# Kernel tuning notes

Measured on AMD Instinct MI355X. Metric: run time of the kernel, lower is better.

The kernel has to match this reference:

```python
import jax, jax.numpy as jnp
import numpy as np
import math

N_KEYS = 2048      # set size (number of pragma keys)
EMB = 768          # embed_size
KEY_E = 512        # key_embed_size
VAL_E = 256        # val_embed_size (KEY_E + VAL_E == EMB)
CAT_VOCAB = 100000 # categorical embedding rows
N_REG = 1000       # integer-key embedding rows / per-key Linear(1,256) encoders
HID = 512          # hidden_size (dim_V)
HEADS = 8
N_OUT = 7          # PMA num_outputs
SCALE = math.sqrt(HID)  # original divides by sqrt(dim_V), not sqrt(head_dim)


def _split_heads(x):
    # torch: torch.cat(x.split(dim_V//h, 2), 0)  -> [h*B, N, dim_V/h]
    return jnp.concatenate(jnp.split(x, HEADS, axis=2), axis=0)


def _merge_heads(x):
    # torch: torch.cat(x.split(B, 0), 2)
    return jnp.concatenate(jnp.split(x, HEADS, axis=0), axis=2)


def _mab(Q, K, wq, bq, wk, bk, wv, bv, wo, bo):
    # MAB with ln=False: project, head-split along batch, attend, residual, relu FF residual
    Qp = Q @ wq.T + bq
    Kp = K @ wk.T + bk
    Vp = K @ wv.T + bv
    Q_, K_, V_ = _split_heads(Qp), _split_heads(Kp), _split_heads(Vp)
    A = jax.nn.softmax(jnp.einsum('bqd,bkd->bqk', Q_, K_) / SCALE, axis=-1)
    O = _merge_heads(Q_ + jnp.einsum('bqk,bkd->bqd', A, V_))
    return O + jax.nn.relu(O @ wo.T + bo)


def _forward(reg_values, cat_table, reg_table, reg_W, reg_b,
             q0_w, q0_b, k0_w, k0_b, v0_w, v0_b, o0_w, o0_b,
             qs_w, qs_b, ks_w, ks_b, vs_w, vs_b, os_w, os_b,
             S, pq_w, pq_b, pk_w, pk_b, pv_w, pv_b, po_w, po_b,
             fc_w, fc_b, is_cat, cat_idx, reg_idx):
    # vectorized form of the per-key python loop: gather -> tiny linear encode -> select
    val_emb = reg_W[reg_idx] * reg_values[:, None] + reg_b[reg_idx]     # [N, VAL_E]
    reg_full = jnp.concatenate([reg_table[reg_idx], val_emb], axis=-1)  # [N, EMB]
    emb = jnp.where(is_cat[:, None], cat_table[cat_idx], reg_full)[None]  # [1, N, EMB]
    x = _mab(emb, emb, q0_w, q0_b, k0_w, k0_b, v0_w, v0_b, o0_w, o0_b)
    for i in range(3):
        x = _mab(x, x, qs_w[i], qs_b[i], ks_w[i], ks_b[i], vs_w[i], vs_b[i], os_w[i], os_b[i])
    # decoder: PMA (MAB(S, X)) then Linear(HID, 1)
    s = jnp.broadcast_to(S, (x.shape[0], N_OUT, HID))
    p = _mab(s, x, pq_w, pq_b, pk_w, pk_b, pv_w, pv_b, po_w, po_b)      # [1, N_OUT, HID]
    return (p @ fc_w.T + fc_b).reshape(-1)                              # [N_OUT]


def setup_inputs() -> dict:
    key = jax.random.key(0)
    ks = iter(jax.random.split(key, 48))
    def w(shape, s=0.02):
        return jax.random.normal(next(ks), shape, jnp.float32) * s
    inp = {}
    inp['is_cat'] = jax.random.bernoulli(next(ks), 0.5, (N_KEYS,))
    inp['cat_idx'] = jax.random.randint(next(ks), (N_KEYS,), 0, CAT_VOCAB)
    inp['reg_idx'] = jax.random.randint(next(ks), (N_KEYS,), 0, N_REG)
    inp['reg_values'] = jax.random.uniform(next(ks), (N_KEYS,), jnp.float32, 1.0, 64.0)
    inp['cat_table'] = w((CAT_VOCAB, EMB), 0.05)
    inp['reg_table'] = w((N_REG, KEY_E), 0.05)
    inp['reg_W'] = w((N_REG, VAL_E))
    inp['reg_b'] = w((N_REG, VAL_E))
    inp['q0_w'] = w((HID, EMB)); inp['q0_b'] = w((HID,))
    inp['k0_w'] = w((HID, EMB)); inp['k0_b'] = w((HID,))
    inp['v0_w'] = w((HID, EMB)); inp['v0_b'] = w((HID,))
    inp['o0_w'] = w((HID, HID)); inp['o0_b'] = w((HID,))
    for nm in ['qs', 'ks', 'vs', 'os']:
        inp[nm + '_w'] = w((3, HID, HID))
        inp[nm + '_b'] = w((3, HID))
    inp['S'] = w((1, N_OUT, HID), 0.05)
    for nm in ['pq', 'pk', 'pv', 'po']:
        inp[nm + '_w'] = w((HID, HID))
        inp[nm + '_b'] = w((HID,))
    inp['fc_w'] = w((1, HID)); inp['fc_b'] = w((1,))
    return inp


def reference(is_cat, cat_idx, reg_idx, reg_values, cat_table, reg_table, reg_W, reg_b,
              q0_w, q0_b, k0_w, k0_b, v0_w, v0_b, o0_w, o0_b,
              qs_w, qs_b, ks_w, ks_b, vs_w, vs_b, os_w, os_b,
              S, pq_w, pq_b, pk_w, pk_b, pv_w, pv_b, po_w, po_b, fc_w, fc_b):
    return _forward(reg_values, cat_table, reg_table, reg_W, reg_b,
                    q0_w, q0_b, k0_w, k0_b, v0_w, v0_b, o0_w, o0_b,
                    qs_w, qs_b, ks_w, ks_b, vs_w, vs_b, os_w, os_b,
                    S, pq_w, pq_b, pk_w, pk_b, pv_w, pv_b, po_w, po_b,
                    fc_w, fc_b, is_cat, cat_idx, reg_idx)
```

## Files before the change

kernel.cpp:

```cpp
#include <hip/hip_runtime.h>
#include <stdint.h>


#define HID 512
#define EMBD 768
#define NCTX 2048
#define HD 64

typedef __attribute__((ext_vector_type(8))) short v8s;
typedef __attribute__((ext_vector_type(4))) float v4f;

#define MFMA(a, b, c) __builtin_amdgcn_mfma_f32_16x16x32_bf16((a), (b), (c), 0, 0, 0)

__device__ __forceinline__ short f2bf(float f) {
  uint32_t u = __builtin_bit_cast(uint32_t, f);
  uint32_t r = (u + 0x7FFFu + ((u >> 16) & 1u)) >> 16;
  return (short)r;
}
__device__ __forceinline__ float bf2f(short s) {
  uint32_t u = ((uint32_t)(uint16_t)s) << 16;
  return __builtin_bit_cast(float, u);
}
__device__ __forceinline__ v8s ldbf8(const short* p) { return *(const v8s*)p; }

struct ConvDesc {
  const float* src[20];
  unsigned cum[21];
};

__global__ void k_convert(ConvDesc d, short* __restrict__ dst) {
  unsigned i = blockIdx.x * 256u + threadIdx.x;
  if (i >= d.cum[20]) return;
  int t = 0;
  while (i >= d.cum[t + 1]) ++t;
  dst[i] = f2bf(d.src[t][i - d.cum[t]]);
}

__global__ void k_emb(const int* __restrict__ is_cat, const int* __restrict__ cat_idx,
                      const int* __restrict__ reg_idx, const float* __restrict__ reg_values,
                      const float* __restrict__ cat_table, const float* __restrict__ reg_table,
                      const float* __restrict__ reg_W, const float* __restrict__ reg_b,
                      short* __restrict__ out) {
  int i = blockIdx.x * 256 + threadIdx.x;
  int n = i / EMBD, e = i - n * EMBD;
  float v;
  if (is_cat[n]) {
    v = cat_table[(long)cat_idx[n] * EMBD + e];
  } else {
    int r = reg_idx[n];
    if (e < 512) v = reg_table[r * 512 + e];
    else {
      int e2 = e - 512;
      v = reg_W[r * 256 + e2] * reg_values[n] + reg_b[r * 256 + e2];
    }
  }
  out[i] = f2bf(v);
}

__global__ void k_sbuild(const float* __restrict__ S, short* __restrict__ out) {
  int i = blockIdx.x * 256 + threadIdx.x;
  int row = i >> 9;
  out[i] = (row < 7) ? f2bf(S[i]) : (short)0;
}

template <int EPI, int KK>
__global__ __launch_bounds__(64) void k_gemm(const short* __restrict__ A,
                                             const short* __restrict__ B,
                                             const float* __restrict__ biasA,
                                             const float* __restrict__ biasB,
                                             const short* __restrict__ resid,
                                             short* __restrict__ out, int N) {
  int l = threadIdx.x, l16 = l & 15, quad = l >> 4;
  int i0 = blockIdx.y * 16, n0 = blockIdx.x * 64;
  const short* arow = A + (i0 + l16) * KK + quad * 8;
  const short* brow = B + (n0 + l16) * KK + quad * 8;
  v4f acc[4];
  for (int t = 0; t < 4; ++t) acc[t] = (v4f){0.f, 0.f, 0.f, 0.f};
#pragma unroll 2
  for (int k = 0; k < KK; k += 32) {
    v8s a = ldbf8(arow + k);
    acc[0] = MFMA(a, ldbf8(brow + k), acc[0]);
    acc[1] = MFMA(a, ldbf8(brow + 16 * KK + k), acc[1]);
    acc[2] = MFMA(a, ldbf8(brow + 32 * KK + k), acc[2]);
    acc[3] = MFMA(a, ldbf8(brow + 48 * KK + k), acc[3]);
  }
  for (int t = 0; t < 4; ++t) {
    int col = n0 + t * 16 + l16;
    float bc;
    if (EPI == 0) bc = (col < 512) ? biasA[col] : biasB[col - 512];
    else if (EPI == 2) bc = biasA[col];
    else bc = 0.f;
    for (int r = 0; r < 4; ++r) {
      int row = i0 + quad * 4 + r;
      float v = acc[t][r];
      if (EPI == 0) v += bc;
      else if (EPI == 1) v += biasA[row];
      else v = bf2f(resid[row * N + col]) + fmaxf(v + bc, 0.f);
      out[row * N + col] = f2bf(v);
    }
  }
}

__global__ __launch_bounds__(256) void k_flash(const short* __restrict__ Q, int qstride,
                                               const short* __restrict__ Kp, int kstride,
                                               const short* __restrict__ Vt,
                                               short* __restrict__ out) {
  __shared__ __align__(16) short Kt[64 * 64];
  __shared__ __align__(16) short Vtl[64 * 64];
  __shared__ __align__(16) short P[4][16 * 72];
  const int tid = threadIdx.x;
  const int wave = tid >> 6, l = tid & 63, l16 = l & 15, quad = l >> 4;
  const int D0 = blockIdx.y * HD;
  const int i0 = blockIdx.x * 64 + wave * 16;

  const short* qrow = Q + (i0 + l16) * qstride + D0 + quad * 8;
  const v8s aq0 = ldbf8(qrow);
  const v8s aq1 = ldbf8(qrow + 32);

  const int sr = tid >> 2, sc0 = tid & 3, sc1 = sc0 + 4;
  const short* kg = Kp + sr * kstride + D0;
  const short* vg = Vt + (D0 + sr) * NCTX;
  short* kl0 = &Kt[(sr * 8 + (sc0 ^ (sr & 7))) * 8];
  short* kl1 = &Kt[(sr * 8 + (sc1 ^ (sr & 7))) * 8];
  short* vl0 = &Vtl[(sr * 8 + (sc0 ^ (sr & 7))) * 8];
  short* vl1 = &Vtl[(sr * 8 + (sc1 ^ (sr & 7))) * 8];

  v4f o[4];
  float lsum[4];
  for (int t = 0; t < 4; ++t) o[t] = (v4f){0.f, 0.f, 0.f, 0.f};
  for (int r = 0; r < 4; ++r) lsum[r] = 0.f;

  v8s pk0 = ldbf8(kg + sc0 * 8), pk1 = ldbf8(kg + sc1 * 8);
  v8s pv0 = ldbf8(vg + sc0 * 8), pv1 = ldbf8(vg + sc1 * 8);

  const float C2 = 0.06375872f;

  for (int j0 = 0; j0 < NCTX; j0 += 64) {
    __syncthreads();
    *(v8s*)kl0 = pk0; *(v8s*)kl1 = pk1;
    *(v8s*)vl0 = pv0; *(v8s*)vl1 = pv1;
    __syncthreads();
    int jn = j0 + 64;
    if (jn < NCTX) {
      pk0 = ldbf8(kg + jn * kstride + sc0 * 8);
      pk1 = ldbf8(kg + jn * kstride + sc1 * 8);
      pv0 = ldbf8(vg + jn + sc0 * 8);
      pv1 = ldbf8(vg + jn + sc1 * 8);
    }
    v4f s[4];
    for (int kt = 0; kt < 4; ++kt) {
      int R = kt * 16 + l16;
      v8s kb0 = *(const v8s*)&Kt[(R * 8 + (quad ^ (R & 7))) * 8];
      v8s kb1 = *(const v8s*)&Kt[(R * 8 + ((quad + 4) ^ (R & 7))) * 8];
      v4f t0 = (v4f){0.f, 0.f, 0.f, 0.f};
      t0 = MFMA(aq0, kb0, t0);
      s[kt] = MFMA(aq1, kb1, t0);
    }
    short* pw = &P[wave][0];
    for (int kt = 0; kt < 4; ++kt)
      for (int r = 0; r < 4; ++r) {
        float p = exp2f(fminf(s[kt][r] * C2, 40.f));
        lsum[r] += p;
        pw[(quad * 4 + r) * 72 + kt * 16 + l16] = f2bf(p);
      }
    __syncthreads();
    v8s pa0 = *(const v8s*)&pw[l16 * 72 + quad * 8];
    v8s pa1 = *(const v8s*)&pw[l16 * 72 + 32 + quad * 8];
    for (int t = 0; t < 4; ++t) {
      int R = t * 16 + l16;
      v8s bv0 = *(const v8s*)&Vtl[(R * 8 + (quad ^ (R & 7))) * 8];
      v8s bv1 = *(const v8s*)&Vtl[(R * 8 + ((quad + 4) ^ (R & 7))) * 8];
      o[t] = MFMA(pa0, bv0, o[t]);
      o[t] = MFMA(pa1, bv1, o[t]);
    }
  }
  for (int r = 0; r < 4; ++r) {
    lsum[r] += __shfl_xor(lsum[r], 1);
    lsum[r] += __shfl_xor(lsum[r], 2);
    lsum[r] += __shfl_xor(lsum[r], 4);
    lsum[r] += __shfl_xor(lsum[r], 8);
  }
  for (int r = 0; r < 4; ++r) {
    float inv = 1.f / lsum[r];
    int row = i0 + quad * 4 + r;
    for (int t = 0; t < 4; ++t) {
      int col = D0 + t * 16 + l16;
      out[row * HID + col] = f2bf(bf2f(Q[row * qstride + col]) + o[t][r] * inv);
    }
  }
}

__global__ __launch_bounds__(64) void k_fc(const short* __restrict__ P,
                                           const float* __restrict__ fcw,
                                           const float* __restrict__ fcb,
                                           float* __restrict__ out) {
  int j = blockIdx.x, l = threadIdx.x;
  float s = 0.f;
  int d0 = l * 8;
  for (int d = d0; d < d0 + 8; ++d) s += bf2f(P[j * HID + d]) * fcw[d];
  for (int msk = 1; msk < 64; msk <<= 1) s += __shfl_xor(s, msk);
  if (l == 0) out[j] = s + fcb[0];
}

extern "C" void kernel_launch(void* const* d_in, const int* in_sizes, int n_in,
                              void* d_out, int out_size, void* d_ws, size_t ws_size,
                              hipStream_t stream) {
  const int* is_cat = (const int*)d_in[0];
  const int* cat_idx = (const int*)d_in[1];
  const int* reg_idx = (const int*)d_in[2];
  const float* reg_values = (const float*)d_in[3];
  const float* cat_table = (const float*)d_in[4];
  const float* reg_table = (const float*)d_in[5];
  const float* reg_W = (const float*)d_in[6];
  const float* reg_b = (const float*)d_in[7];
  const float* q0_w = (const float*)d_in[8];  const float* q0_b = (const float*)d_in[9];
  const float* k0_w = (const float*)d_in[10]; const float* k0_b = (const float*)d_in[11];
  const float* v0_w = (const float*)d_in[12]; const float* v0_b = (const float*)d_in[13];
  const float* o0_w = (const float*)d_in[14]; const float* o0_b = (const float*)d_in[15];
  const float* qs_w = (const float*)d_in[16]; const float* qs_b = (const float*)d_in[17];
  const float* ks_w = (const float*)d_in[18]; const float* ks_b = (const float*)d_in[19];
  const float* vs_w = (const float*)d_in[20]; const float* vs_b = (const float*)d_in[21];
  const float* os_w = (const float*)d_in[22]; const float* os_b = (const float*)d_in[23];
  const float* S    = (const float*)d_in[24];
  const float* pq_w = (const float*)d_in[25]; const float* pq_b = (const float*)d_in[26];
  const float* pk_w = (const float*)d_in[27]; const float* pk_b = (const float*)d_in[28];
  const float* pv_w = (const float*)d_in[29]; const float* pv_b = (const float*)d_in[30];
  const float* po_w = (const float*)d_in[31]; const float* po_b = (const float*)d_in[32];
  const float* fc_w = (const float*)d_in[33]; const float* fc_b = (const float*)d_in[34];

  short* W = (short*)d_ws;

  const unsigned OWQK[4] = {0u, 1441792u, 2490368u, 3538944u};
  const unsigned OWV[4]  = {786432u, 1966080u, 3014656u, 4063232u};
  const unsigned OWO[4]  = {1179648u, 2228224u, 3276800u, 4325376u};
  const unsigned OPQW = 4587520u, OPKW = 4849664u, OPVW = 5111808u, OPOW = 5373952u;
  const unsigned TOTW = 5636096u;
  const unsigned OEMB = TOTW;
  const unsigned OXA  = OEMB + 1572864u;
  const unsigned OXB  = OXA + 1048576u;
  const unsigned OQK  = OXB + 1048576u;
  const unsigned OVT  = OQK + 2097152u;
  const unsigned OOH  = OVT + 1048576u;
  const unsigned OSB  = OOH + 1048576u;
  const unsigned OQPP = OSB + 32768u;
  const unsigned OKPP = OQPP + 32768u;
  const unsigned OOHP = OKPP + 1048576u;
  const unsigned OPP  = OOHP + 32768u;

  ConvDesc cd;
  const float* srcs[20] = {
      q0_w, k0_w, v0_w, o0_w,
      qs_w, ks_w, vs_w, os_w,
      qs_w + 262144, ks_w + 262144, vs_w + 262144, os_w + 262144,
      qs_w + 524288, ks_w + 524288, vs_w + 524288, os_w + 524288,
      pq_w, pk_w, pv_w, po_w};
  const unsigned cums[21] = {0u,       393216u,  786432u,  1179648u, 1441792u,
                             1703936u, 1966080u, 2228224u, 2490368u, 2752512u,
                             3014656u, 3276800u, 3538944u, 3801088u, 4063232u,
                             4325376u, 4587520u, 4849664u, 5111808u, 5373952u,
                             5636096u};
  for (int i = 0; i < 20; ++i) cd.src[i] = srcs[i];
  for (int i = 0; i < 21; ++i) cd.cum[i] = cums[i];
  k_convert<<<(TOTW + 255) / 256, 256, 0, stream>>>(cd, W);

  k_emb<<<(2048 * 768) / 256, 256, 0, stream>>>(is_cat, cat_idx, reg_idx, reg_values,
                                                cat_table, reg_table, reg_W, reg_b,
                                                W + OEMB);
  k_sbuild<<<(64 * 512) / 256, 256, 0, stream>>>(S, W + OSB);

  const float* bq[4] = {q0_b, qs_b, qs_b + 512, qs_b + 1024};
  const float* bk[4] = {k0_b, ks_b, ks_b + 512, ks_b + 1024};
  const float* bv[4] = {v0_b, vs_b, vs_b + 512, vs_b + 1024};
  const float* bo[4] = {o0_b, os_b, os_b + 512, os_b + 1024};
  const unsigned oxin[4]  = {OEMB, OXA, OXB, OXA};
  const unsigned oxout[4] = {OXA, OXB, OXA, OXB};

  dim3 gqk(16, 128);
  dim3 gv(32, 32);
  dim3 go(8, 128);
  dim3 gf(32, 8);

  for (int l = 0; l < 4; ++l) {
    const short* X = W + oxin[l];
    short* Xout = W + oxout[l];
    if (l == 0) {
      k_gemm<0, 768><<<gqk, 64, 0, stream>>>(X, W + OWQK[0], bq[0], bk[0], nullptr, W + OQK, 1024);
      k_gemm<1, 768><<<gv, 64, 0, stream>>>(W + OWV[0], X, bv[0], bv[0], nullptr, W + OVT, 2048);
    } else {
      k_gemm<0, 512><<<gqk, 64, 0, stream>>>(X, W + OWQK[l], bq[l], bk[l], nullptr, W + OQK, 1024);
      k_gemm<1, 512><<<gv, 64, 0, stream>>>(W + OWV[l], X, bv[l], bv[l], nullptr, W + OVT, 2048);
    }
    k_flash<<<gf, 256, 0, stream>>>(W + OQK, 1024, W + OQK + 512, 1024, W + OVT, W + OOH);
    k_gemm<2, 512><<<go, 64, 0, stream>>>(W + OOH, W + OWO[l], bo[l], bo[l], W + OOH, Xout, 512);
  }

  k_gemm<0, 512><<<dim3(8, 4), 64, 0, stream>>>(W + OSB, W + OPQW, pq_b, pq_b, nullptr, W + OQPP, 512);
  k_gemm<0, 512><<<dim3(8, 128), 64, 0, stream>>>(W + OXB, W + OPKW, pk_b, pk_b, nullptr, W + OKPP, 512);
  k_gemm<1, 512><<<dim3(32, 32), 64, 0, stream>>>(W + OPVW, W + OXB, pv_b, pv_b, nullptr, W + OVT, 2048);
  k_flash<<<dim3(1, 8), 256, 0, stream>>>(W + OQPP, 512, W + OKPP, 512, W + OVT, W + OOHP);
  k_gemm<2, 512><<<dim3(8, 1), 64, 0, stream>>>(W + OOHP, W + OPOW, po_b, po_b, W + OOHP, W + OPP, 512);
  k_fc<<<7, 64, 0, stream>>>(W + OPP, fc_w, fc_b, (float*)d_out);
}
```

Measured before the change: 833.8 us.

## Split attention over key chunks with combine kernel and enlarge GEMM row tiles

The flash attention kernel now splits the 2048-key loop into 4 chunks along a new grid z dimension. Each chunk writes unnormalized fp32 partial outputs and row sums, and a new k_combine kernel sums the partials, normalizes them and adds the residual. This gives four times as many workgroups for a grid that previously filled only about one block per CU. The GEMM kernel now computes 32 rows per wave, two A fragments sharing each B load, which halves the grid sizes and reduces B reloads. The per-wave P buffer handoff uses an LDS waitcnt instead of a block barrier. The cost is an extra launch and fp32 partial traffic per layer.

```diff
diff --git a/kernel.cpp b/kernel.cpp
--- a/kernel.cpp
+++ b/kernel.cpp
@@ -71,55 +71,63 @@
                                              const short* __restrict__ resid,
                                              short* __restrict__ out, int N) {
   int l = threadIdx.x, l16 = l & 15, quad = l >> 4;
-  int i0 = blockIdx.y * 16, n0 = blockIdx.x * 64;
-  const short* arow = A + (i0 + l16) * KK + quad * 8;
-  const short* brow = B + (n0 + l16) * KK + quad * 8;
-  v4f acc[4];
-  for (int t = 0; t < 4; ++t) acc[t] = (v4f){0.f, 0.f, 0.f, 0.f};
-#pragma unroll 2
+  int i0 = blockIdx.y * 32, n0 = blockIdx.x * 64;
+  const short* a0p = A + (i0 + l16) * KK + quad * 8;
+  const short* a1p = a0p + 16 * KK;
+  const short* bp = B + (n0 + l16) * KK + quad * 8;
+  v4f acc[2][4];
+  for (int g = 0; g < 2; ++g)
+    for (int t = 0; t < 4; ++t) acc[g][t] = (v4f){0.f, 0.f, 0.f, 0.f};
+#pragma unroll 4
   for (int k = 0; k < KK; k += 32) {
-    v8s a = ldbf8(arow + k);
-    acc[0] = MFMA(a, ldbf8(brow + k), acc[0]);
-    acc[1] = MFMA(a, ldbf8(brow + 16 * KK + k), acc[1]);
-    acc[2] = MFMA(a, ldbf8(brow + 32 * KK + k), acc[2]);
-    acc[3] = MFMA(a, ldbf8(brow + 48 * KK + k), acc[3]);
-  }
-  for (int t = 0; t < 4; ++t) {
-    int col = n0 + t * 16 + l16;
-    float bc;
-    if (EPI == 0) bc = (col < 512) ? biasA[col] : biasB[col - 512];
-    else if (EPI == 2) bc = biasA[col];
-    else bc = 0.f;
-    for (int r = 0; r < 4; ++r) {
-      int row = i0 + quad * 4 + r;
-      float v = acc[t][r];
-      if (EPI == 0) v += bc;
-      else if (EPI == 1) v += biasA[row];
-      else v = bf2f(resid[row * N + col]) + fmaxf(v + bc, 0.f);
-      out[row * N + col] = f2bf(v);
-    }
-  }
+    v8s a0 = ldbf8(a0p + k);
+    v8s a1 = ldbf8(a1p + k);
+#pragma unroll
+    for (int t = 0; t < 4; ++t) {
+      v8s b = ldbf8(bp + t * 16 * KK + k);
+      acc[0][t] = MFMA(a0, b, acc[0][t]);
+      acc[1][t] = MFMA(a1, b, acc[1][t]);
+    }
+  }
+  for (int g = 0; g < 2; ++g)
+    for (int t = 0; t < 4; ++t) {
+      int col = n0 + t * 16 + l16;
+      float bc;
+      if (EPI == 0) bc = (col < 512) ? biasA[col] : biasB[col - 512];
+      else if (EPI == 2) bc = biasA[col];
+      else bc = 0.f;
+      for (int r = 0; r < 4; ++r) {
+        int row = i0 + g * 16 + quad * 4 + r;
+        float v = acc[g][t][r];
+        if (EPI == 0) v += bc;
+        else if (EPI == 1) v += biasA[row];
+        else v = bf2f(resid[row * N + col]) + fmaxf(v + bc, 0.f);
+        out[row * N + col] = f2bf(v);
+      }
+    }
 }
 
 __global__ __launch_bounds__(256) void k_flash(const short* __restrict__ Q, int qstride,
                                                const short* __restrict__ Kp, int kstride,
                                                const short* __restrict__ Vt,
-                                               short* __restrict__ out) {
+                                               float* __restrict__ opart,
+                                               float* __restrict__ lspart) {
   __shared__ __align__(16) short Kt[64 * 64];
   __shared__ __align__(16) short Vtl[64 * 64];
   __shared__ __align__(16) short P[4][16 * 72];
   const int tid = threadIdx.x;
   const int wave = tid >> 6, l = tid & 63, l16 = l & 15, quad = l >> 4;
-  const int D0 = blockIdx.y * HD;
+  const int h = blockIdx.y, D0 = h * HD;
   const int i0 = blockIdx.x * 64 + wave * 16;
+  const int z = blockIdx.z, jbase = z * (NCTX / 4);
 
   const short* qrow = Q + (i0 + l16) * qstride + D0 + quad * 8;
   const v8s aq0 = ldbf8(qrow);
   const v8s aq1 = ldbf8(qrow + 32);
 
   const int sr = tid >> 2, sc0 = tid & 3, sc1 = sc0 + 4;
-  const short* kg = Kp + sr * kstride + D0;
-  const short* vg = Vt + (D0 + sr) * NCTX;
+  const short* kg = Kp + (jbase + sr) * kstride + D0;
+  const short* vg = Vt + (D0 + sr) * NCTX + jbase;
   short* kl0 = &Kt[(sr * 8 + (sc0 ^ (sr & 7))) * 8];
   short* kl1 = &Kt[(sr * 8 + (sc1 ^ (sr & 7))) * 8];
   short* vl0 = &Vtl[(sr * 8 + (sc0 ^ (sr & 7))) * 8];
@@ -135,19 +143,20 @@
 
   const float C2 = 0.06375872f;
 
-  for (int j0 = 0; j0 < NCTX; j0 += 64) {
+  for (int j0 = 0; j0 < NCTX / 4; j0 += 64) {
     __syncthreads();
     *(v8s*)kl0 = pk0; *(v8s*)kl1 = pk1;
     *(v8s*)vl0 = pv0; *(v8s*)vl1 = pv1;
     __syncthreads();
     int jn = j0 + 64;
-    if (jn < NCTX) {
+    if (jn < NCTX / 4) {
       pk0 = ldbf8(kg + jn * kstride + sc0 * 8);
       pk1 = ldbf8(kg + jn * kstride + sc1 * 8);
       pv0 = ldbf8(vg + jn + sc0 * 8);
       pv1 = ldbf8(vg + jn + sc1 * 8);
     }
     v4f s[4];
+#pragma unroll
     for (int kt = 0; kt < 4; ++kt) {
       int R = kt * 16 + l16;
       v8s kb0 = *(const v8s*)&Kt[(R * 8 + (quad ^ (R & 7))) * 8];
@@ -157,15 +166,17 @@
       s[kt] = MFMA(aq1, kb1, t0);
     }
     short* pw = &P[wave][0];
+#pragma unroll
     for (int kt = 0; kt < 4; ++kt)
       for (int r = 0; r < 4; ++r) {
         float p = exp2f(fminf(s[kt][r] * C2, 40.f));
         lsum[r] += p;
         pw[(quad * 4 + r) * 72 + kt * 16 + l16] = f2bf(p);
       }
-    __syncthreads();
+    asm volatile("s_waitcnt lgkmcnt(0)" ::: "memory");
     v8s pa0 = *(const v8s*)&pw[l16 * 72 + quad * 8];
     v8s pa1 = *(const v8s*)&pw[l16 * 72 + 32 + quad * 8];
+#pragma unroll
     for (int t = 0; t < 4; ++t) {
       int R = t * 16 + l16;
       v8s bv0 = *(const v8s*)&Vtl[(R * 8 + (quad ^ (R & 7))) * 8];
@@ -180,14 +191,25 @@
     lsum[r] += __shfl_xor(lsum[r], 4);
     lsum[r] += __shfl_xor(lsum[r], 8);
   }
-  for (int r = 0; r < 4; ++r) {
-    float inv = 1.f / lsum[r];
-    int row = i0 + quad * 4 + r;
-    for (int t = 0; t < 4; ++t) {
-      int col = D0 + t * 16 + l16;
-      out[row * HID + col] = f2bf(bf2f(Q[row * qstride + col]) + o[t][r] * inv);
-    }
-  }
+  float* ob = opart + (size_t)z * (NCTX * HID);
+  for (int t = 0; t < 4; ++t)
+    for (int r = 0; r < 4; ++r)
+      ob[(i0 + quad * 4 + r) * HID + D0 + t * 16 + l16] = o[t][r];
+  if (l16 == 0)
+    for (int r = 0; r < 4; ++r)
+      lspart[z * (8 * NCTX) + h * NCTX + i0 + quad * 4 + r] = lsum[r];
+}
+
+__global__ void k_combine(const float* __restrict__ op, const float* __restrict__ ls,
+                          const short* __restrict__ Qr, int qstride,
+                          short* __restrict__ out) {
+  const int PS = NCTX * HID;
+  int i = blockIdx.x * 256 + threadIdx.x;
+  int row = i >> 9, col = i & 511, h = col >> 6;
+  float o = op[i] + op[i + PS] + op[i + 2 * PS] + op[i + 3 * PS];
+  int li = h * NCTX + row;
+  float d = ls[li] + ls[li + 8 * NCTX] + ls[li + 16 * NCTX] + ls[li + 24 * NCTX];
+  out[i] = f2bf(bf2f(Qr[row * qstride + col]) + o / d);
 }
 
 __global__ __launch_bounds__(64) void k_fc(const short* __restrict__ P,
@@ -246,6 +268,9 @@
   const unsigned OKPP = OQPP + 32768u;
   const unsigned OOHP = OKPP + 1048576u;
   const unsigned OPP  = OOHP + 32768u;
+  const unsigned OF32 = OPP + 32768u;
+  float* F = (float*)(W + OF32);
+  float* LS = F + 4u * 1048576u;
 
   ConvDesc cd;
   const float* srcs[20] = {
@@ -275,10 +300,10 @@
   const unsigned oxin[4]  = {OEMB, OXA, OXB, OXA};
   const unsigned oxout[4] = {OXA, OXB, OXA, OXB};
 
-  dim3 gqk(16, 128);
-  dim3 gv(32, 32);
-  dim3 go(8, 128);
-  dim3 gf(32, 8);
+  dim3 gqk(16, 64);
+  dim3 gv(32, 16);
+  dim3 go(8, 64);
+  dim3 gf(32, 8, 4);
 
   for (int l = 0; l < 4; ++l) {
     const short* X = W + oxin[l];
@@ -290,14 +315,16 @@
       k_gemm<0, 512><<<gqk, 64, 0, stream>>>(X, W + OWQK[l], bq[l], bk[l], nullptr, W + OQK, 1024);
       k_gemm<1, 512><<<gv, 64, 0, stream>>>(W + OWV[l], X, bv[l], bv[l], nullptr, W + OVT, 2048);
     }
-    k_flash<<<gf, 256, 0, stream>>>(W + OQK, 1024, W + OQK + 512, 1024, W + OVT, W + OOH);
+    k_flash<<<gf, 256, 0, stream>>>(W + OQK, 1024, W + OQK + 512, 1024, W + OVT, F, LS);
+    k_combine<<<(2048 * 512) / 256, 256, 0, stream>>>(F, LS, W + OQK, 1024, W + OOH);
     k_gemm<2, 512><<<go, 64, 0, stream>>>(W + OOH, W + OWO[l], bo[l], bo[l], W + OOH, Xout, 512);
   }
 
-  k_gemm<0, 512><<<dim3(8, 4), 64, 0, stream>>>(W + OSB, W + OPQW, pq_b, pq_b, nullptr, W + OQPP, 512);
-  k_gemm<0, 512><<<dim3(8, 128), 64, 0, stream>>>(W + OXB, W + OPKW, pk_b, pk_b, nullptr, W + OKPP, 512);
-  k_gemm<1, 512><<<dim3(32, 32), 64, 0, stream>>>(W + OPVW, W + OXB, pv_b, pv_b, nullptr, W + OVT, 2048);
-  k_flash<<<dim3(1, 8), 256, 0, stream>>>(W + OQPP, 512, W + OKPP, 512, W + OVT, W + OOHP);
+  k_gemm<0, 512><<<dim3(8, 2), 64, 0, stream>>>(W + OSB, W + OPQW, pq_b, pq_b, nullptr, W + OQPP, 512);
+  k_gemm<0, 512><<<dim3(8, 64), 64, 0, stream>>>(W + OXB, W + OPKW, pk_b, pk_b, nullptr, W + OKPP, 512);
+  k_gemm<1, 512><<<dim3(32, 16), 64, 0, stream>>>(W + OPVW, W + OXB, pv_b, pv_b, nullptr, W + OVT, 2048);
+  k_flash<<<dim3(1, 8, 4), 256, 0, stream>>>(W + OQPP, 512, W + OKPP, 512, W + OVT, F, LS);
+  k_combine<<<(16 * 512) / 256, 256, 0, stream>>>(F, LS, W + OQPP, 512, W + OOHP);
   k_gemm<2, 512><<<dim3(8, 1), 64, 0, stream>>>(W + OOHP, W + OPOW, po_b, po_b, W + OOHP, W + OPP, 512);
   k_fc<<<7, 64, 0, stream>>>(W + OPP, fc_w, fc_b, (float*)d_out);
 }
```

After: 742.3 us. 11.0% less time.
